# Kernel tuning notes

Measured on AMD Instinct MI355X. Metric: run time of the kernel, lower is better.

## Reference

```python
import jax, jax.numpy as jnp
import numpy as np

BN_EPS = 1e-5
DIM = 256
RED = 4
KH, KW = 3, 3


def setup_inputs() -> dict:
    key = jax.random.key(0)
    ks = jax.random.split(key, 4)
    b, c, h, w = 32, DIM, 64, 64
    hid = DIM // RED
    x = jax.random.normal(ks[0], (b, c, h, w), dtype=jnp.float32)
    # 1x1 convs are just matmuls on pooled [b, c] vectors; store as [out, in]
    w1 = jax.random.normal(ks[1], (hid, c), dtype=jnp.float32) * (1.0 / np.sqrt(c))
    bn_gamma = jnp.ones((hid,), dtype=jnp.float32)
    bn_beta = jnp.zeros((hid,), dtype=jnp.float32)
    bn_mean = jnp.zeros((hid,), dtype=jnp.float32)
    bn_var = jnp.ones((hid,), dtype=jnp.float32)
    w2 = jax.random.normal(ks[2], (c * KH * KW, hid), dtype=jnp.float32) * (1.0 / np.sqrt(hid))
    b2 = jnp.zeros((c * KH * KW,), dtype=jnp.float32)
    bias = jnp.zeros((c,), dtype=jnp.float32)
    return {"x": x, "w1": w1, "bn_gamma": bn_gamma, "bn_beta": bn_beta,
            "bn_mean": bn_mean, "bn_var": bn_var, "w2": w2, "b2": b2, "bias": bias}


def reference(x, w1, bn_gamma, bn_beta, bn_mean, bn_var, w2, b2, bias):
    b, c, h, w = x.shape
    # --- SE-style dynamic weight generation ---
    pooled = jnp.mean(x, axis=(2, 3))                      # [b, c]
    y = jnp.einsum('bc,rc->br', pooled, w1)                # conv1 (1x1, no bias)
    y = (y - bn_mean) * jax.lax.rsqrt(bn_var + BN_EPS) * bn_gamma + bn_beta
    y = jax.nn.sigmoid(y)                                  # note: relu is defined but unused in forward
    dyn = jnp.einsum('br,kr->bk', y, w2) + b2              # [b, c*KH*KW]
    dyn = dyn.reshape(b * c, 1, KH, KW)                    # per-sample depthwise kernels (OIHW)
    # --- per-sample depthwise conv via batch-as-groups trick ---
    out = jax.lax.conv_general_dilated(
        x.reshape(1, b * c, h, w), dyn,
        window_strides=(1, 1), padding=((1, 1), (1, 1)),
        feature_group_count=b * c,
        dimension_numbers=('NCHW', 'OIHW', 'NCHW'))
    out = out.reshape(b, c, h, w) + bias[None, :, None, None]
    return out
```

## Files before the change

kernel.cpp:

```cpp
#include <hip/hip_runtime.h>

#define DIM 256
#define HID 64
#define HW 4096
#define LW 72

typedef float f4 __attribute__((ext_vector_type(4)));

__device__ __forceinline__ int skew_of(int R) {
    int r3 = R & 3;
    int g = (r3 & 2) ? r3 : 0;
    return ((R >> 2) + g) & 3;
}

__global__ __launch_bounds__(256) void pool_kernel(const float* __restrict__ x,
                                                   float* __restrict__ pooled) {
    int plane = blockIdx.x;
    const float4* p = (const float4*)(x + (size_t)plane * HW);
    int tid = threadIdx.x;
    float s = 0.f;
#pragma unroll
    for (int k = 0; k < 4; ++k) {
        float4 v = p[tid + k * 256];
        s += (v.x + v.y) + (v.z + v.w);
    }
#pragma unroll
    for (int off = 32; off > 0; off >>= 1) s += __shfl_down(s, off, 64);
    __shared__ float ws[4];
    int wid = tid >> 6, lane = tid & 63;
    if (lane == 0) ws[wid] = s;
    __syncthreads();
    if (tid == 0) {
        float t = (ws[0] + ws[1]) + (ws[2] + ws[3]);
        pooled[plane] = t * (1.0f / (float)HW);
    }
}

__global__ __launch_bounds__(64) void sig_kernel(const float* __restrict__ pooled,
                                                 const float* __restrict__ w1,
                                                 const float* __restrict__ gamma,
                                                 const float* __restrict__ beta,
                                                 const float* __restrict__ mean,
                                                 const float* __restrict__ var,
                                                 float* __restrict__ sigg) {
    int b = blockIdx.x;
    int t = threadIdx.x;
    __shared__ float sp[DIM];
    ((float4*)sp)[t] = ((const float4*)(pooled + b * DIM))[t];
    __syncthreads();
    const float4* wr = (const float4*)(w1 + t * DIM);
    const float4* s4 = (const float4*)sp;
    float acc = 0.f;
#pragma unroll
    for (int i = 0; i < DIM / 4; ++i) {
        float4 v = wr[i]; float4 u = s4[i];
        acc += v.x * u.x + v.y * u.y + v.z * u.z + v.w * u.w;
    }
    float yb = (acc - mean[t]) * rsqrtf(var[t] + 1e-5f) * gamma[t] + beta[t];
    sigg[b * HID + t] = 1.0f / (1.0f + expf(-yb));
}

__global__ __launch_bounds__(256) void conv_kernel(const float* __restrict__ x,
                                                   const float* __restrict__ sigg,
                                                   const float* __restrict__ w2,
                                                   const float* __restrict__ b2,
                                                   const float* __restrict__ bias,
                                                   float* __restrict__ out) {
    int plane = 8191 - (int)blockIdx.x;
    int c = plane & (DIM - 1);
    int b = plane >> 8;
    int tid = threadIdx.x;
    const float* xp = x + (size_t)plane * HW;

    __shared__ float lds[66 * LW];
    __shared__ float wsh[12];

    const f4* xp4 = (const f4*)xp;
    f4 st[4];
#pragma unroll
    for (int k = 0; k < 4; ++k) st[k] = __builtin_nontemporal_load(&xp4[tid + k * 256]);

    if (tid < 9) {
        int kk = c * 9 + tid;
        const float4* wk = (const float4*)(w2 + (size_t)kk * HID);
        const float4* sg = (const float4*)(sigg + b * HID);
        float acc = b2[kk];
#pragma unroll
        for (int i = 0; i < HID / 4; ++i) {
            float4 v = wk[i]; float4 u = sg[i];
            acc += v.x * u.x + v.y * u.y + v.z * u.z + v.w * u.w;
        }
        wsh[tid] = acc;
    }

    for (int i = tid; i < 272; i += 256) {
        int addr;
        if (i < 72)        addr = i;
        else if (i < 144)  addr = 65 * LW + (i - 72);
        else {
            int z = i - 144;
            int R = 1 + (z >> 1);
            addr = R * LW + skew_of(R) + 3 + (z & 1) * 65;
        }
        lds[addr] = 0.f;
    }

#pragma unroll
    for (int k = 0; k < 4; ++k) {
        int idx = tid + k * 256;
        int R = (idx >> 4) + 1;
        int col0 = (idx & 15) * 4;
        float* dst = &lds[R * LW + skew_of(R) + 4 + col0];
        dst[0] = st[k].x; dst[1] = st[k].y; dst[2] = st[k].z; dst[3] = st[k].w;
    }
    __syncthreads();

    float w[9];
#pragma unroll
    for (int i = 0; i < 9; ++i) w[i] = wsh[i];
    float bv = bias[c];

    int u = tid >> 4, j = tid & 15;
    float acc[4][4];
#pragma unroll
    for (int m = 0; m < 4; ++m)
#pragma unroll
        for (int i = 0; i < 4; ++i) acc[m][i] = bv;

#define FCT(m, t)                                                              \
    {                                                                          \
        float w0 = w[(t)*3 + 0], w1v = w[(t)*3 + 1], w2v = w[(t)*3 + 2];       \
        acc[m][0] += w0 * a0 + w1v * a1 + w2v * a2;                            \
        acc[m][1] += w0 * a1 + w1v * a2 + w2v * a3;                            \
        acc[m][2] += w0 * a2 + w1v * a3 + w2v * a4;                            \
        acc[m][3] += w0 * a3 + w1v * a4 + w2v * a5;                            \
    }
#define FRD(d)                                                                 \
    float a0, a1, a2, a3, a4, a5;                                              \
    {                                                                          \
        int R = 4 * u + (d);                                                   \
        const float* r = &lds[R * LW + skew_of(R) + 3 + 4 * j];                \
        a0 = r[0]; a1 = r[1]; a2 = r[2]; a3 = r[3]; a4 = r[4]; a5 = r[5];      \
    }

    { FRD(0) FCT(0, 0) }
    { FRD(1) FCT(0, 1) FCT(1, 0) }
    { FRD(2) FCT(0, 2) FCT(1, 1) FCT(2, 0) }
    { FRD(3) FCT(1, 2) FCT(2, 1) FCT(3, 0) }
    { FRD(4) FCT(2, 2) FCT(3, 1) }
    { FRD(5) FCT(3, 2) }
#undef FRD
#undef FCT

    f4* op4 = (f4*)(out + (size_t)plane * HW);
#pragma unroll
    for (int m = 0; m < 4; ++m) {
        f4 o;
        o.x = acc[m][0]; o.y = acc[m][1]; o.z = acc[m][2]; o.w = acc[m][3];
        __builtin_nontemporal_store(o, &op4[(4 * u + m) * 16 + j]);
    }
}

extern "C" void kernel_launch(void* const* d_in, const int* in_sizes, int n_in,
                              void* d_out, int out_size, void* d_ws, size_t ws_size,
                              hipStream_t stream) {
    const float* x     = (const float*)d_in[0];
    const float* w1    = (const float*)d_in[1];
    const float* gamma = (const float*)d_in[2];
    const float* beta  = (const float*)d_in[3];
    const float* mean  = (const float*)d_in[4];
    const float* var   = (const float*)d_in[5];
    const float* w2    = (const float*)d_in[6];
    const float* b2    = (const float*)d_in[7];
    const float* bias  = (const float*)d_in[8];
    float* out = (float*)d_out;

    float* pooled = (float*)d_ws;
    float* sigg = pooled + 8192;

    pool_kernel<<<8192, 256, 0, stream>>>(x, pooled);
    sig_kernel<<<32, 64, 0, stream>>>(pooled, w1, gamma, beta, mean, var, sigg);
    conv_kernel<<<8192, 256, 0, stream>>>(x, sigg, w2, b2, bias, out);
}
```

Baseline: 72.20 us.

## Fuse pooling and sigmoid stages with atomic counters, drop reversed conv block order

Merges the pooling kernel and the small SE/sigmoid kernel into one launch. 32 extra tail blocks spin on per-batch atomic counters until all 256 planes of their batch are pooled, then compute the sigmoid vector. A memset to clear the counters is added. The conv kernel's reversed block order, which likely aimed to reuse L2-resident planes written last by pooling, is removed. This trades one launch for a memset plus spin-wait, and relies on tail blocks being scheduled after the producers.

```diff
diff --git a/kernel.cpp b/kernel.cpp
--- a/kernel.cpp
+++ b/kernel.cpp
@@ -13,51 +13,63 @@
     return ((R >> 2) + g) & 3;
 }
 
-__global__ __launch_bounds__(256) void pool_kernel(const float* __restrict__ x,
-                                                   float* __restrict__ pooled) {
-    int plane = blockIdx.x;
-    const float4* p = (const float4*)(x + (size_t)plane * HW);
+__global__ __launch_bounds__(256) void pool_sig_kernel(const float* __restrict__ x,
+                                                       const float* __restrict__ w1,
+                                                       const float* __restrict__ gamma,
+                                                       const float* __restrict__ beta,
+                                                       const float* __restrict__ mean,
+                                                       const float* __restrict__ var,
+                                                       float* __restrict__ pooled,
+                                                       float* __restrict__ sigg,
+                                                       unsigned int* __restrict__ cnt) {
+    int bid = blockIdx.x;
     int tid = threadIdx.x;
-    float s = 0.f;
+    __shared__ float ws[4];
+    __shared__ __align__(16) float sp[DIM];
+
+    if (bid < 8192) {
+        int plane = bid;
+        const float4* p = (const float4*)(x + (size_t)plane * HW);
+        float s = 0.f;
 #pragma unroll
-    for (int k = 0; k < 4; ++k) {
-        float4 v = p[tid + k * 256];
-        s += (v.x + v.y) + (v.z + v.w);
+        for (int k = 0; k < 4; ++k) {
+            float4 v = p[tid + k * 256];
+            s += (v.x + v.y) + (v.z + v.w);
+        }
+#pragma unroll
+        for (int off = 32; off > 0; off >>= 1) s += __shfl_down(s, off, 64);
+        int wid = tid >> 6, lane = tid & 63;
+        if (lane == 0) ws[wid] = s;
+        __syncthreads();
+        if (tid == 0) {
+            float t = (ws[0] + ws[1]) + (ws[2] + ws[3]);
+            float val = t * (1.0f / (float)HW);
+            float old = atomicExch(&pooled[plane], val);
+            asm volatile("" :: "v"(old) : "memory");
+            atomicAdd(&cnt[plane >> 8], 1u);
+        }
+        return;
     }
+
+    int b = bid - 8192;
+    if (tid == 0) {
+        while (atomicAdd(&cnt[b], 0u) < 256u) { __builtin_amdgcn_s_sleep(2); }
+    }
+    __syncthreads();
+    sp[tid] = atomicAdd(&pooled[b * DIM + tid], 0.0f);
+    __syncthreads();
+    if (tid < HID) {
+        const f4* wr = (const f4*)(w1 + (size_t)tid * DIM);
+        const f4* s4 = (const f4*)sp;
+        float acc = 0.f;
 #pragma unroll
-    for (int off = 32; off > 0; off >>= 1) s += __shfl_down(s, off, 64);
-    __shared__ float ws[4];
-    int wid = tid >> 6, lane = tid & 63;
-    if (lane == 0) ws[wid] = s;
-    __syncthreads();
-    if (tid == 0) {
-        float t = (ws[0] + ws[1]) + (ws[2] + ws[3]);
-        pooled[plane] = t * (1.0f / (float)HW);
+        for (int i = 0; i < DIM / 4; ++i) {
+            f4 v = wr[i], u_ = s4[i];
+            acc += v.x * u_.x + v.y * u_.y + v.z * u_.z + v.w * u_.w;
+        }
+        float yb = (acc - mean[tid]) * rsqrtf(var[tid] + 1e-5f) * gamma[tid] + beta[tid];
+        sigg[b * HID + tid] = 1.0f / (1.0f + expf(-yb));
     }
-}
-
-__global__ __launch_bounds__(64) void sig_kernel(const float* __restrict__ pooled,
-                                                 const float* __restrict__ w1,
-                                                 const float* __restrict__ gamma,
-                                                 const float* __restrict__ beta,
-                                                 const float* __restrict__ mean,
-                                                 const float* __restrict__ var,
-                                                 float* __restrict__ sigg) {
-    int b = blockIdx.x;
-    int t = threadIdx.x;
-    __shared__ float sp[DIM];
-    ((float4*)sp)[t] = ((const float4*)(pooled + b * DIM))[t];
-    __syncthreads();
-    const float4* wr = (const float4*)(w1 + t * DIM);
-    const float4* s4 = (const float4*)sp;
-    float acc = 0.f;
-#pragma unroll
-    for (int i = 0; i < DIM / 4; ++i) {
-        float4 v = wr[i]; float4 u = s4[i];
-        acc += v.x * u.x + v.y * u.y + v.z * u.z + v.w * u.w;
-    }
-    float yb = (acc - mean[t]) * rsqrtf(var[t] + 1e-5f) * gamma[t] + beta[t];
-    sigg[b * HID + t] = 1.0f / (1.0f + expf(-yb));
 }
 
 __global__ __launch_bounds__(256) void conv_kernel(const float* __restrict__ x,
@@ -66,7 +78,7 @@
                                                    const float* __restrict__ b2,
                                                    const float* __restrict__ bias,
                                                    float* __restrict__ out) {
-    int plane = 8191 - (int)blockIdx.x;
+    int plane = blockIdx.x;
     int c = plane & (DIM - 1);
     int b = plane >> 8;
     int tid = threadIdx.x;
@@ -176,9 +188,11 @@
     float* out = (float*)d_out;
 
     float* pooled = (float*)d_ws;
-    float* sigg = pooled + 8192;
+    float* sigg   = pooled + 8192;
+    unsigned int* cnt = (unsigned int*)(sigg + 2048);
 
-    pool_kernel<<<8192, 256, 0, stream>>>(x, pooled);
-    sig_kernel<<<32, 64, 0, stream>>>(pooled, w1, gamma, beta, mean, var, sigg);
+    hipMemsetAsync(cnt, 0, 32 * sizeof(unsigned int), stream);
+    pool_sig_kernel<<<8224, 256, 0, stream>>>(x, w1, gamma, beta, mean, var,
+                                              pooled, sigg, cnt);
     conv_kernel<<<8192, 256, 0, stream>>>(x, sigg, w2, b2, bias, out);
 }
```

Result: slower. 143.3 us (+98.4%).
